# Kernel tuning notes

Hardware: AMD Instinct MI355X
Metric: run time of the kernel (lower is better)

## Reference

```python
import jax, jax.numpy as jnp
import numpy as np

B, C, T, H = 2, 1024, 2048, 16
D = C // H  # head dim = 64


def setup_inputs() -> dict:
    key = jax.random.key(0)
    ks = jax.random.split(key, 10)
    s = 1.0 / np.sqrt(C).astype(np.float32)
    x = jax.random.normal(ks[0], (B, C, T), jnp.float32)
    mask = jax.random.randint(ks[1], (B, 1, T), 0, 2).astype(bool)
    Wq = jax.random.normal(ks[2], (C, C), jnp.float32) * s
    bq = jax.random.normal(ks[3], (C,), jnp.float32) * 0.02
    Wk = jax.random.normal(ks[4], (C, C), jnp.float32) * s
    bk = jax.random.normal(ks[5], (C,), jnp.float32) * 0.02
    Wv = jax.random.normal(ks[6], (C, C), jnp.float32) * s
    bv = jax.random.normal(ks[7], (C,), jnp.float32) * 0.02
    Wp = jax.random.normal(ks[8], (C, C), jnp.float32) * s
    bp = jax.random.normal(ks[9], (C,), jnp.float32) * 0.02
    return {"x": x, "mask": mask, "Wq": Wq, "bq": bq, "Wk": Wk, "bk": bk,
            "Wv": Wv, "bv": bv, "Wp": Wp, "bp": bp}


def _conv1x1(W, b, z):
    # Conv1d with kernel size 1 == per-position GEMM over channels.
    return jnp.einsum('oc,bct->bot', W, z) + b[None, :, None]


def reference(x, mask, Wq, bq, Wk, bk, Wv, bv, Wp, bp):
    b_, c_, t_ = x.shape
    scale = 1.0 / np.sqrt(D).astype(np.float32)
    q = _conv1x1(Wq, bq, x)
    k = _conv1x1(Wk, bk, x)
    v = _conv1x1(Wv, bv, x)
    # [B, C, T] -> [B, H, T, D]  (view(B,H,D,T).transpose(2,3))
    q = q.reshape(b_, H, D, t_).transpose(0, 1, 3, 2)
    k = k.reshape(b_, H, D, t_).transpose(0, 1, 3, 2)
    v = v.reshape(b_, H, D, t_).transpose(0, 1, 3, 2)
    att = jnp.einsum('bhqd,bhkd->bhqk', q * scale, k)
    m = mask[:, :, None, :]  # [B,1,1,T] key mask
    att = jnp.where(m, att, -jnp.inf)
    p = jax.nn.softmax(att, axis=-1)
    p = jnp.where(m, p, 0.0)
    vm = v * mask[:, :, :, None].astype(v.dtype)  # zero masked values
    out = jnp.einsum('bhqk,bhkd->bhqd', p, vm)
    # [B,H,T,D] -> [B,C,T]
    out = out.transpose(0, 1, 3, 2).reshape(b_, c_, t_)
    out = _conv1x1(Wp, bp, out) * mask.astype(out.dtype)
    return (out, mask)
```

## Files before the change

### kernel.cpp

```cpp
#include <hip/hip_runtime.h>

typedef unsigned short u16;
typedef unsigned int u32;
typedef short bf16x8 __attribute__((ext_vector_type(8)));
typedef float f32x4 __attribute__((ext_vector_type(4)));

constexpr int Bb = 2, Cc = 1024, Tt = 2048, Hh = 16, Dd = 64;

__device__ __forceinline__ u16 f2bf(float f) {
    union { float f; u32 i; } c; c.f = f;
    u32 u = c.i;
    u32 r = (u + 0x7FFFu + ((u >> 16) & 1u)) >> 16;
    return (u16)r;
}
__device__ __forceinline__ u32 pk_bf2(float lo, float hi) {
    union { float f; u32 i; } a, b; a.f = lo; b.f = hi;
    u32 ua = a.i + 0x8000u, ub = b.i + 0x8000u;
    return (ub & 0xFFFF0000u) | (ua >> 16);
}
__device__ __forceinline__ u32 scl2(u32 w) {
    union { float f; u32 i; } lo, hi;
    lo.i = w << 16; hi.i = w & 0xFFFF0000u;
    lo.f *= 0.125f; hi.f *= 0.125f;
    return (hi.i & 0xFFFF0000u) | (lo.i >> 16);
}
__device__ __forceinline__ void gl_lds16(const u16* g, u16* l) {
    __builtin_amdgcn_global_load_lds(
        (const __attribute__((address_space(1))) u32*)(const void*)g,
        (__attribute__((address_space(3))) u32*)(void*)l, 16, 0, 0);
}

__global__ __launch_bounds__(256) void prep(const int* __restrict__ mask,
                                            int* __restrict__ pfx,
                                            int* __restrict__ tmap,
                                            int* __restrict__ nk,
                                            const float* __restrict__ w0,
                                            const float* __restrict__ w1,
                                            const float* __restrict__ w2,
                                            const float* __restrict__ w3,
                                            u16* __restrict__ wout) {
    if (blockIdx.x < 2) {
        __shared__ int part[256];
        int b = blockIdx.x;
        const int* m = mask + b * Tt;
        int t8 = threadIdx.x * 8;
        int v[8], s = 0;
#pragma unroll
        for (int i = 0; i < 8; i++) { v[i] = m[t8 + i] ? 1 : 0; s += v[i]; }
        part[threadIdx.x] = s;
        __syncthreads();
        for (int off = 1; off < 256; off <<= 1) {
            int val = (threadIdx.x >= off) ? part[threadIdx.x - off] : 0;
            __syncthreads();
            part[threadIdx.x] += val;
            __syncthreads();
        }
        int run = part[threadIdx.x] - s;
#pragma unroll
        for (int i = 0; i < 8; i++) {
            pfx[b * Tt + t8 + i] = run;
            if (v[i]) { tmap[b * Tt + run] = t8 + i; run++; }
        }
        if (threadIdx.x == 255) nk[b] = part[255];
    } else {
        int bi = blockIdx.x - 2;
        int wsel = bi >> 10, blk = bi & 1023;
        const float* in = (wsel == 0) ? w0 : (wsel == 1) ? w1 : (wsel == 2) ? w2 : w3;
        u16* o = wout + (size_t)wsel * Cc * Cc;
        int i = (blk * 256 + threadIdx.x) * 4;
        float4 v = *(const float4*)(in + i);
        o[i + 0] = f2bf(v.x);
        o[i + 1] = f2bf(v.y);
        o[i + 2] = f2bf(v.z);
        o[i + 3] = f2bf(v.w);
    }
}

__global__ __launch_bounds__(256) void transpose_x(const float* __restrict__ x,
                                                   const int* __restrict__ mask,
                                                   const int* __restrict__ pfx,
                                                   u16* __restrict__ xT) {
    __shared__ u16 tile[32][33];
    int b = blockIdx.z;
    int t0 = blockIdx.x * 32, c0 = blockIdx.y * 32;
    int tx = threadIdx.x, ty = threadIdx.y;
    const float* xb = x + (size_t)b * Cc * Tt;
    u16* xTb = xT + (size_t)b * Tt * Cc;
#pragma unroll
    for (int i = 0; i < 4; i++) {
        int r = ty + i * 8;
        tile[r][tx] = f2bf(xb[(size_t)(c0 + r) * Tt + t0 + tx]);
    }
    __syncthreads();
#pragma unroll
    for (int i = 0; i < 4; i++) {
        int r = ty + i * 8;
        int t = t0 + r;
        if (mask[b * Tt + t]) {
            int slot = pfx[b * Tt + t];
            xTb[(size_t)slot * Cc + c0 + tx] = tile[tx][r];
        }
    }
}

__global__ __launch_bounds__(256) void gemm_qkv(const u16* __restrict__ A,
                                                const u16* __restrict__ Bt,
                                                const float* __restrict__ b0,
                                                const float* __restrict__ b1,
                                                const float* __restrict__ b2,
                                                const int* __restrict__ nk,
                                                u16* __restrict__ qb, u16* __restrict__ kb,
                                                u16* __restrict__ vT) {
    constexpr int K = Cc;
    __shared__ u16 Alds[128 * 64];
    __shared__ u16 Blds[128 * 64];
    int n0 = blockIdx.x * 128, m0 = blockIdx.y * 128;
    int bb = m0 >> 11;
    if ((m0 & 2047) >= nk[bb]) return;
    int tid = threadIdx.x;
    int lane = tid & 63, wave = tid >> 6;
    int quad = lane >> 4, id15 = lane & 15;
    int wm0 = (wave & 1) * 64, wn0 = (wave >> 1) * 64;
    int srow = lane >> 3;
    int scol = ((lane & 7) ^ srow) * 8;
    int sw = id15 & 7;

    f32x4 acc[4][4] = {};

    for (int k0 = 0; k0 < K; k0 += 64) {
        __syncthreads();
#pragma unroll
        for (int t = 0; t < 4; t++) {
            int g = wave * 4 + t;
            int r = g * 8 + srow;
            gl_lds16(A + (size_t)(m0 + r) * K + k0 + scol, &Alds[g * 512]);
            gl_lds16(Bt + (size_t)(n0 + r) * K + k0 + scol, &Blds[g * 512]);
        }
        __syncthreads();
#pragma unroll
        for (int hf = 0; hf < 2; hf++) {
            bf16x8 af[4], bf[4];
#pragma unroll
            for (int i = 0; i < 4; i++) {
                int c = (((hf << 2) | quad) ^ sw) * 8;
                af[i] = *(const bf16x8*)(&Alds[(wm0 + i * 16 + id15) * 64 + c]);
                bf[i] = *(const bf16x8*)(&Blds[(wn0 + i * 16 + id15) * 64 + c]);
            }
#pragma unroll
            for (int ni = 0; ni < 4; ni++)
#pragma unroll
                for (int mi = 0; mi < 4; mi++)
                    acc[ni][mi] = __builtin_amdgcn_mfma_f32_16x16x32_bf16(
                        bf[ni], af[mi], acc[ni][mi], 0, 0, 0);
        }
    }

    int mt0 = (m0 & 2047) + wm0;
#pragma unroll
    for (int ni = 0; ni < 4; ni++) {
        int nr = n0 + wn0 + ni * 16 + quad * 4;
        int sect = nr >> 10;
        int nn = nr & 1023;
        int h = nn >> 6, d0 = nn & 63;
        const float* bp_ = (sect == 0) ? b0 : (sect == 1) ? b1 : b2;
        float4 bv4 = *(const float4*)(bp_ + nn);
        if (sect < 2) {
            u16* dst = ((sect == 0) ? qb : kb) + ((size_t)bb * Hh + h) * Tt * (size_t)Dd;
#pragma unroll
            for (int mi = 0; mi < 4; mi++) {
                int mt = mt0 + mi * 16 + id15;
                uint2 w;
                w.x = pk_bf2(acc[ni][mi][0] + bv4.x, acc[ni][mi][1] + bv4.y);
                w.y = pk_bf2(acc[ni][mi][2] + bv4.z, acc[ni][mi][3] + bv4.w);
                *(uint2*)(dst + (size_t)mt * Dd + d0) = w;
            }
        } else {
            u16* dst = vT + ((size_t)bb * Hh + h) * Dd * (size_t)Tt;
#pragma unroll
            for (int mi = 0; mi < 4; mi++) {
                int mt = mt0 + mi * 16 + id15;
                dst[(size_t)(d0 + 0) * Tt + mt] = f2bf(acc[ni][mi][0] + bv4.x);
                dst[(size_t)(d0 + 1) * Tt + mt] = f2bf(acc[ni][mi][1] + bv4.y);
                dst[(size_t)(d0 + 2) * Tt + mt] = f2bf(acc[ni][mi][2] + bv4.z);
                dst[(size_t)(d0 + 3) * Tt + mt] = f2bf(acc[ni][mi][3] + bv4.w);
            }
        }
    }
}

__global__ __launch_bounds__(256) void gemm_proj(const u16* __restrict__ A,
                                                 const u16* __restrict__ Bt,
                                                 const float* __restrict__ b0,
                                                 const int* __restrict__ mask,
                                                 float* __restrict__ out,
                                                 float* __restrict__ outTail) {
    constexpr int K = Cc;
    __shared__ u16 Alds[128 * 64];
    __shared__ u16 Blds[64 * 64];
    int n0 = blockIdx.x * 64, m0 = blockIdx.y * 128;
    int tid = threadIdx.x;
    if (outTail && blockIdx.x == 0 && blockIdx.y == 0) {
        for (int i = tid; i < Bb * Tt; i += 256) outTail[i] = mask[i] ? 1.0f : 0.0f;
    }
    int lane = tid & 63, wave = tid >> 6;
    int quad = lane >> 4, id15 = lane & 15;
    int wn0 = (wave & 1) * 32, wm0 = (wave >> 1) * 64;
    int srow = lane >> 3;
    int scol = ((lane & 7) ^ srow) * 8;
    int sw = id15 & 7;

    f32x4 acc[2][4] = {};

    for (int k0 = 0; k0 < K; k0 += 64) {
        __syncthreads();
#pragma unroll
        for (int t = 0; t < 4; t++) {
            int g = wave * 4 + t;
            gl_lds16(A + (size_t)(m0 + g * 8 + srow) * K + k0 + scol, &Alds[g * 512]);
        }
#pragma unroll
        for (int t = 0; t < 2; t++) {
            int g = wave * 2 + t;
            gl_lds16(Bt + (size_t)(n0 + g * 8 + srow) * K + k0 + scol, &Blds[g * 512]);
        }
        __syncthreads();
#pragma unroll
        for (int hf = 0; hf < 2; hf++) {
            bf16x8 af[4], bf[2];
            int c = (((hf << 2) | quad) ^ sw) * 8;
#pragma unroll
            for (int i = 0; i < 4; i++)
                af[i] = *(const bf16x8*)(&Alds[(wm0 + i * 16 + id15) * 64 + c]);
#pragma unroll
            for (int i = 0; i < 2; i++)
                bf[i] = *(const bf16x8*)(&Blds[(wn0 + i * 16 + id15) * 64 + c]);
#pragma unroll
            for (int ni = 0; ni < 2; ni++)
#pragma unroll
                for (int mi = 0; mi < 4; mi++)
                    acc[ni][mi] = __builtin_amdgcn_mfma_f32_16x16x32_bf16(
                        bf[ni], af[mi], acc[ni][mi], 0, 0, 0);
        }
    }

    int bb = m0 >> 11;
    int mt0 = (m0 & 2047) + wm0;
#pragma unroll
    for (int ni = 0; ni < 2; ni++) {
        int nr = n0 + wn0 + ni * 16 + quad * 4;
        float4 bv4 = *(const float4*)(b0 + nr);
#pragma unroll
        for (int mi = 0; mi < 4; mi++) {
            int m = mt0 + mi * 16 + id15;
            int mg = (bb << 11) + m;
            float mm = (float)mask[mg];
            float* o = out + ((size_t)bb * Cc + nr) * Tt + m;
            o[0 * Tt] = (acc[ni][mi][0] + bv4.x) * mm;
            o[1 * Tt] = (acc[ni][mi][1] + bv4.y) * mm;
            o[2 * Tt] = (acc[ni][mi][2] + bv4.z) * mm;
            o[3 * Tt] = (acc[ni][mi][3] + bv4.w) * mm;
        }
    }
}

__global__ __launch_bounds__(256) void attn(const u16* __restrict__ q,
                                            const u16* __restrict__ kk,
                                            const u16* __restrict__ vT,
                                            const int* __restrict__ tmap,
                                            const int* __restrict__ nk,
                                            u16* __restrict__ o_buf) {
    __shared__ u16 Kl[2][128 * 64];
    __shared__ u16 Vl[2][64 * 128];
    int bh = blockIdx.y;
    int b = bh >> 4, h = bh & 15;
    int t0 = blockIdx.x * 64;
    int nkb = nk[b];
    if (t0 >= nkb) return;
    int tid = threadIdx.x;
    int lane = tid & 63, wave = tid >> 6;
    int quad = lane >> 4, id15 = lane & 15;
    int wq = t0 + wave * 16;
    const u16* qb = q + (size_t)bh * Tt * Dd;
    const u16* kb = kk + (size_t)bh * Tt * Dd;
    const u16* vb = vT + (size_t)bh * Dd * Tt;

    union { uint4 r; bf16x8 v; } qf[2];
#pragma unroll
    for (int hf = 0; hf < 2; hf++) {
        uint4 r = *(const uint4*)(qb + (size_t)(wq + id15) * Dd + hf * 32 + quad * 8);
        qf[hf].r.x = scl2(r.x);
        qf[hf].r.y = scl2(r.y);
        qf[hf].r.z = scl2(r.z);
        qf[hf].r.w = scl2(r.w);
    }

    int srowK = lane >> 3;
    int scolK = ((lane & 7) ^ srowK) * 8;
    int srowV = lane >> 4;
    int sw = id15 & 7;

    float l = 0.0f;
    f32x4 accO[4] = {};

#pragma unroll
    for (int t = 0; t < 4; t++) {
        int g = wave * 4 + t;
        gl_lds16(kb + (size_t)(g * 8 + srowK) * Dd + scolK, &Kl[0][g * 512]);
        int d = g * 4 + srowV;
        int sc = (lane & 15) ^ (4 * (g & 1) + srowV);
        gl_lds16(vb + (size_t)d * Tt + sc * 8, &Vl[0][g * 512]);
    }

    int shA = ((quad & 1) * 2) * 16 + id15;
    int shB = shA + 16;

    int cbuf = 0;
    for (int j0 = 0; j0 < nkb; j0 += 128, cbuf ^= 1) {
        __syncthreads();
        if (j0 + 128 < nkb) {
            int bn = cbuf ^ 1, jn = j0 + 128;
#pragma unroll
            for (int t = 0; t < 4; t++) {
                int g = wave * 4 + t;
                gl_lds16(kb + (size_t)(jn + g * 8 + srowK) * Dd + scolK, &Kl[bn][g * 512]);
                int d = g * 4 + srowV;
                int sc = (lane & 15) ^ (4 * (g & 1) + srowV);
                gl_lds16(vb + (size_t)d * Tt + jn + sc * 8, &Vl[bn][g * 512]);
            }
        }
        const u16* Kb = Kl[cbuf];
        const u16* Vb = Vl[cbuf];

        f32x4 st[8] = {};
#pragma unroll
        for (int kt = 0; kt < 8; kt++) {
            int krow = kt * 16 + id15;
#pragma unroll
            for (int hf = 0; hf < 2; hf++) {
                bf16x8 kf = *(const bf16x8*)(Kb + krow * 64 + (((hf << 2) | quad) ^ sw) * 8);
                st[kt] = __builtin_amdgcn_mfma_f32_16x16x32_bf16(kf, qf[hf].v, st[kt], 0, 0, 0);
            }
        }

        if (j0 + 128 > nkb) {
#pragma unroll
            for (int kt = 0; kt < 8; kt++) {
                int jb = j0 + kt * 16 + quad * 4;
#pragma unroll
                for (int r = 0; r < 4; r++)
                    if (jb + r >= nkb) st[kt][r] = -1e30f;
            }
        }

        u32 pkk[4][2][2];
#pragma unroll
        for (int kt = 0; kt < 8; kt++) {
            float p0 = __expf(st[kt][0]);
            float p1 = __expf(st[kt][1]);
            float p2 = __expf(st[kt][2]);
            float p3 = __expf(st[kt][3]);
            l += (p0 + p1) + (p2 + p3);
            pkk[kt >> 1][kt & 1][0] = pk_bf2(p0, p1);
            pkk[kt >> 1][kt & 1][1] = pk_bf2(p2, p3);
        }

#pragma unroll
        for (int g = 0; g < 4; g++) {
            union { u32 u[4]; bf16x8 v; } pf;
            u32 a0 = (u32)__shfl((int)pkk[g][0][0], shA);
            u32 a1 = (u32)__shfl((int)pkk[g][0][1], shA);
            u32 a2 = (u32)__shfl((int)pkk[g][0][0], shB);
            u32 a3 = (u32)__shfl((int)pkk[g][0][1], shB);
            u32 c0 = (u32)__shfl((int)pkk[g][1][0], shA);
            u32 c1 = (u32)__shfl((int)pkk[g][1][1], shA);
            u32 c2 = (u32)__shfl((int)pkk[g][1][0], shB);
            u32 c3 = (u32)__shfl((int)pkk[g][1][1], shB);
            pf.u[0] = (quad < 2) ? a0 : c0;
            pf.u[1] = (quad < 2) ? a1 : c1;
            pf.u[2] = (quad < 2) ? a2 : c2;
            pf.u[3] = (quad < 2) ? a3 : c3;
#pragma unroll
            for (int dt = 0; dt < 4; dt++) {
                int drow = dt * 16 + id15;
                bf16x8 vf = *(const bf16x8*)(Vb + drow * 128 + (((g << 2) | quad) ^ sw) * 8);
                accO[dt] = __builtin_amdgcn_mfma_f32_16x16x32_bf16(vf, pf.v, accO[dt], 0, 0, 0);
            }
        }
    }

    int slot = wq + id15;
    bool ok = slot < nkb;
    int torig = ok ? tmap[b * Tt + slot] : 0;
    float lv = l;
    lv += __shfl_xor(lv, 16);
    lv += __shfl_xor(lv, 32);
    float inv = 1.0f / lv;
    if (ok) {
#pragma unroll
        for (int dt = 0; dt < 4; dt++) {
            uint2 w;
            w.x = pk_bf2(accO[dt][0] * inv, accO[dt][1] * inv);
            w.y = pk_bf2(accO[dt][2] * inv, accO[dt][3] * inv);
            *(uint2*)(o_buf + ((size_t)b * Tt + torig) * Cc + h * Dd + dt * 16 + quad * 4) = w;
        }
    }
}

extern "C" void kernel_launch(void* const* d_in, const int* in_sizes, int n_in,
                              void* d_out, int out_size, void* d_ws, size_t ws_size,
                              hipStream_t stream) {
    const float* x  = (const float*)d_in[0];
    const int* mask = (const int*)d_in[1];
    const float* Wq = (const float*)d_in[2];
    const float* bq = (const float*)d_in[3];
    const float* Wk = (const float*)d_in[4];
    const float* bk = (const float*)d_in[5];
    const float* Wv = (const float*)d_in[6];
    const float* bv = (const float*)d_in[7];
    const float* Wp = (const float*)d_in[8];
    const float* bp = (const float*)d_in[9];
    float* out = (float*)d_out;

    size_t sz = (size_t)Bb * Tt * Cc;
    size_t wsz = (size_t)Cc * Cc;
    u16* xT = (u16*)d_ws;
    u16* qb = xT + sz;
    u16* kb = qb + sz;
    u16* vT = kb + sz;
    u16* wq16 = vT + sz;
    u16* wp16 = wq16 + 3 * wsz;
    int* pfx  = (int*)(wp16 + wsz);
    int* tmap = pfx + Bb * Tt;
    int* nkp  = tmap + Bb * Tt;
    u16* ob = xT;

    float* outTail = (out_size >= Bb * Cc * Tt + Bb * Tt)
                         ? out + (size_t)Bb * Cc * Tt : nullptr;

    prep<<<2 + 4 * (int)(wsz / 1024), 256, 0, stream>>>(
        mask, pfx, tmap, nkp, Wq, Wk, Wv, Wp, wq16);
    transpose_x<<<dim3(Tt / 32, Cc / 32, Bb), dim3(32, 8), 0, stream>>>(x, mask, pfx, xT);
    gemm_qkv<<<dim3(3 * Cc / 128, Bb * Tt / 128), 256, 0, stream>>>(
        xT, wq16, bq, bk, bv, nkp, qb, kb, vT);
    attn<<<dim3(Tt / 64, Bb * Hh), 256, 0, stream>>>(qb, kb, vT, tmap, nkp, ob);
    gemm_proj<<<dim3(Cc / 64, Bb * Tt / 128), 256, 0, stream>>>(
        ob, wp16, bp, mask, out, outTail);
}
```

Baseline: 186.6 us.

## Shrink GEMM M-tiles and split attention keys across waves for more blocks

Both GEMMs now use 64-row M tiles instead of 128, which doubles the grid size and halves per-wave accumulator work. The attention kernel now handles 32 queries per block and splits the key range into two halves processed by separate wave pairs. The two partial results are merged through LDS before the output is normalised. The aim is more blocks and better CU occupancy for a small problem. In exchange, the attention loop drops K/V double-buffering (loads now stall on syncs), each block redoes more Q/K/V loading, and the split-key merge adds extra syncs.

```diff
diff --git a/kernel.cpp b/kernel.cpp
--- a/kernel.cpp
+++ b/kernel.cpp
@@ -112,44 +112,48 @@
                                                 u16* __restrict__ qb, u16* __restrict__ kb,
                                                 u16* __restrict__ vT) {
     constexpr int K = Cc;
-    __shared__ u16 Alds[128 * 64];
+    __shared__ u16 Alds[64 * 64];
     __shared__ u16 Blds[128 * 64];
-    int n0 = blockIdx.x * 128, m0 = blockIdx.y * 128;
+    int n0 = blockIdx.x * 128, m0 = blockIdx.y * 64;
     int bb = m0 >> 11;
     if ((m0 & 2047) >= nk[bb]) return;
     int tid = threadIdx.x;
     int lane = tid & 63, wave = tid >> 6;
     int quad = lane >> 4, id15 = lane & 15;
-    int wm0 = (wave & 1) * 64, wn0 = (wave >> 1) * 64;
-    int srow = lane >> 3;
-    int scol = ((lane & 7) ^ srow) * 8;
+    int wm0 = (wave & 1) * 32, wn0 = (wave >> 1) * 64;
     int sw = id15 & 7;
 
-    f32x4 acc[4][4] = {};
+    f32x4 acc[4][2] = {};
 
     for (int k0 = 0; k0 < K; k0 += 64) {
         __syncthreads();
 #pragma unroll
-        for (int t = 0; t < 4; t++) {
-            int g = wave * 4 + t;
-            int r = g * 8 + srow;
-            gl_lds16(A + (size_t)(m0 + r) * K + k0 + scol, &Alds[g * 512]);
-            gl_lds16(Bt + (size_t)(n0 + r) * K + k0 + scol, &Blds[g * 512]);
+        for (int i = 0; i < 2; i++) {
+            int s = wave * 128 + i * 64 + lane;
+            int r = s >> 3, c = (s & 7) ^ (r & 7);
+            gl_lds16(A + (size_t)(m0 + r) * K + k0 + c * 8, &Alds[(wave * 128 + i * 64) * 8]);
+        }
+#pragma unroll
+        for (int i = 0; i < 4; i++) {
+            int s = wave * 256 + i * 64 + lane;
+            int r = s >> 3, c = (s & 7) ^ (r & 7);
+            gl_lds16(Bt + (size_t)(n0 + r) * K + k0 + c * 8, &Blds[(wave * 256 + i * 64) * 8]);
         }
         __syncthreads();
 #pragma unroll
         for (int hf = 0; hf < 2; hf++) {
-            bf16x8 af[4], bf[4];
-#pragma unroll
-            for (int i = 0; i < 4; i++) {
-                int c = (((hf << 2) | quad) ^ sw) * 8;
-                af[i] = *(const bf16x8*)(&Alds[(wm0 + i * 16 + id15) * 64 + c]);
-                bf[i] = *(const bf16x8*)(&Blds[(wn0 + i * 16 + id15) * 64 + c]);
-            }
+            int cc = (((hf << 2) | quad) ^ sw) * 8;
+            bf16x8 af[2], bf[4];
+#pragma unroll
+            for (int mi = 0; mi < 2; mi++)
+                af[mi] = *(const bf16x8*)(&Alds[(wm0 + mi * 16 + id15) * 64 + cc]);
 #pragma unroll
             for (int ni = 0; ni < 4; ni++)
-#pragma unroll
-                for (int mi = 0; mi < 4; mi++)
+                bf[ni] = *(const bf16x8*)(&Blds[(wn0 + ni * 16 + id15) * 64 + cc]);
+#pragma unroll
+            for (int ni = 0; ni < 4; ni++)
+#pragma unroll
+                for (int mi = 0; mi < 2; mi++)
                     acc[ni][mi] = __builtin_amdgcn_mfma_f32_16x16x32_bf16(
                         bf[ni], af[mi], acc[ni][mi], 0, 0, 0);
         }
@@ -167,7 +171,7 @@
         if (sect < 2) {
             u16* dst = ((sect == 0) ? qb : kb) + ((size_t)bb * Hh + h) * Tt * (size_t)Dd;
 #pragma unroll
-            for (int mi = 0; mi < 4; mi++) {
+            for (int mi = 0; mi < 2; mi++) {
                 int mt = mt0 + mi * 16 + id15;
                 uint2 w;
                 w.x = pk_bf2(acc[ni][mi][0] + bv4.x, acc[ni][mi][1] + bv4.y);
@@ -177,7 +181,7 @@
         } else {
             u16* dst = vT + ((size_t)bb * Hh + h) * Dd * (size_t)Tt;
 #pragma unroll
-            for (int mi = 0; mi < 4; mi++) {
+            for (int mi = 0; mi < 2; mi++) {
                 int mt = mt0 + mi * 16 + id15;
                 dst[(size_t)(d0 + 0) * Tt + mt] = f2bf(acc[ni][mi][0] + bv4.x);
                 dst[(size_t)(d0 + 1) * Tt + mt] = f2bf(acc[ni][mi][1] + bv4.y);
@@ -195,49 +199,43 @@
                                                  float* __restrict__ out,
                                                  float* __restrict__ outTail) {
     constexpr int K = Cc;
-    __shared__ u16 Alds[128 * 64];
+    __shared__ u16 Alds[64 * 64];
     __shared__ u16 Blds[64 * 64];
-    int n0 = blockIdx.x * 64, m0 = blockIdx.y * 128;
+    int n0 = blockIdx.x * 64, m0 = blockIdx.y * 64;
     int tid = threadIdx.x;
     if (outTail && blockIdx.x == 0 && blockIdx.y == 0) {
         for (int i = tid; i < Bb * Tt; i += 256) outTail[i] = mask[i] ? 1.0f : 0.0f;
     }
     int lane = tid & 63, wave = tid >> 6;
     int quad = lane >> 4, id15 = lane & 15;
-    int wn0 = (wave & 1) * 32, wm0 = (wave >> 1) * 64;
-    int srow = lane >> 3;
-    int scol = ((lane & 7) ^ srow) * 8;
+    int wn0 = (wave & 1) * 32, wm0 = (wave >> 1) * 32;
     int sw = id15 & 7;
 
-    f32x4 acc[2][4] = {};
+    f32x4 acc[2][2] = {};
 
     for (int k0 = 0; k0 < K; k0 += 64) {
         __syncthreads();
 #pragma unroll
-        for (int t = 0; t < 4; t++) {
-            int g = wave * 4 + t;
-            gl_lds16(A + (size_t)(m0 + g * 8 + srow) * K + k0 + scol, &Alds[g * 512]);
-        }
-#pragma unroll
-        for (int t = 0; t < 2; t++) {
-            int g = wave * 2 + t;
-            gl_lds16(Bt + (size_t)(n0 + g * 8 + srow) * K + k0 + scol, &Blds[g * 512]);
+        for (int i = 0; i < 2; i++) {
+            int s = wave * 128 + i * 64 + lane;
+            int r = s >> 3, c = (s & 7) ^ (r & 7);
+            gl_lds16(A + (size_t)(m0 + r) * K + k0 + c * 8, &Alds[(wave * 128 + i * 64) * 8]);
+            gl_lds16(Bt + (size_t)(n0 + r) * K + k0 + c * 8, &Blds[(wave * 128 + i * 64) * 8]);
         }
         __syncthreads();
 #pragma unroll
         for (int hf = 0; hf < 2; hf++) {
-            bf16x8 af[4], bf[2];
-            int c = (((hf << 2) | quad) ^ sw) * 8;
-#pragma unroll
-            for (int i = 0; i < 4; i++)
-                af[i] = *(const bf16x8*)(&Alds[(wm0 + i * 16 + id15) * 64 + c]);
-#pragma unroll
-            for (int i = 0; i < 2; i++)
-                bf[i] = *(const bf16x8*)(&Blds[(wn0 + i * 16 + id15) * 64 + c]);
+            int cc = (((hf << 2) | quad) ^ sw) * 8;
+            bf16x8 af[2], bf[2];
+#pragma unroll
+            for (int i = 0; i < 2; i++) {
+                af[i] = *(const bf16x8*)(&Alds[(wm0 + i * 16 + id15) * 64 + cc]);
+                bf[i] = *(const bf16x8*)(&Blds[(wn0 + i * 16 + id15) * 64 + cc]);
+            }
 #pragma unroll
             for (int ni = 0; ni < 2; ni++)
 #pragma unroll
-                for (int mi = 0; mi < 4; mi++)
+                for (int mi = 0; mi < 2; mi++)
                     acc[ni][mi] = __builtin_amdgcn_mfma_f32_16x16x32_bf16(
                         bf[ni], af[mi], acc[ni][mi], 0, 0, 0);
         }
@@ -250,7 +248,7 @@
         int nr = n0 + wn0 + ni * 16 + quad * 4;
         float4 bv4 = *(const float4*)(b0 + nr);
 #pragma unroll
-        for (int mi = 0; mi < 4; mi++) {
+        for (int mi = 0; mi < 2; mi++) {
             int m = mt0 + mi * 16 + id15;
             int mg = (bb << 11) + m;
             float mm = (float)mask[mg];
@@ -269,17 +267,18 @@
                                             const int* __restrict__ tmap,
                                             const int* __restrict__ nk,
                                             u16* __restrict__ o_buf) {
-    __shared__ u16 Kl[2][128 * 64];
-    __shared__ u16 Vl[2][64 * 128];
+    __shared__ u16 Kl[2][64 * 64];
+    __shared__ u16 Vl[2][64 * 64];
     int bh = blockIdx.y;
     int b = bh >> 4, h = bh & 15;
-    int t0 = blockIdx.x * 64;
+    int t0 = blockIdx.x * 32;
     int nkb = nk[b];
     if (t0 >= nkb) return;
     int tid = threadIdx.x;
     int lane = tid & 63, wave = tid >> 6;
     int quad = lane >> 4, id15 = lane & 15;
-    int wq = t0 + wave * 16;
+    int qg = wave & 1, kh = wave >> 1;
+    int wq = t0 + qg * 16;
     const u16* qb = q + (size_t)bh * Tt * Dd;
     const u16* kb = kk + (size_t)bh * Tt * Dd;
     const u16* vb = vT + (size_t)bh * Dd * Tt;
@@ -294,57 +293,50 @@
         qf[hf].r.w = scl2(r.w);
     }
 
-    int srowK = lane >> 3;
-    int scolK = ((lane & 7) ^ srowK) * 8;
-    int srowV = lane >> 4;
-    int sw = id15 & 7;
+    int nch = (nkb + 63) >> 6;
+    int nch0 = (nch + 1) >> 1;
+    int koff = kh ? nch0 * 64 : 0;
+    int kend = kh ? nkb : ((nch0 * 64 < nkb) ? nch0 * 64 : nkb);
 
     float l = 0.0f;
     f32x4 accO[4] = {};
-
-#pragma unroll
-    for (int t = 0; t < 4; t++) {
-        int g = wave * 4 + t;
-        gl_lds16(kb + (size_t)(g * 8 + srowK) * Dd + scolK, &Kl[0][g * 512]);
-        int d = g * 4 + srowV;
-        int sc = (lane & 15) ^ (4 * (g & 1) + srowV);
-        gl_lds16(vb + (size_t)d * Tt + sc * 8, &Vl[0][g * 512]);
-    }
-
     int shA = ((quad & 1) * 2) * 16 + id15;
     int shB = shA + 16;
-
-    int cbuf = 0;
-    for (int j0 = 0; j0 < nkb; j0 += 128, cbuf ^= 1) {
-        __syncthreads();
-        if (j0 + 128 < nkb) {
-            int bn = cbuf ^ 1, jn = j0 + 128;
-#pragma unroll
-            for (int t = 0; t < 4; t++) {
-                int g = wave * 4 + t;
-                gl_lds16(kb + (size_t)(jn + g * 8 + srowK) * Dd + scolK, &Kl[bn][g * 512]);
-                int d = g * 4 + srowV;
-                int sc = (lane & 15) ^ (4 * (g & 1) + srowV);
-                gl_lds16(vb + (size_t)d * Tt + jn + sc * 8, &Vl[bn][g * 512]);
-            }
-        }
-        const u16* Kb = Kl[cbuf];
-        const u16* Vb = Vl[cbuf];
-
-        f32x4 st[8] = {};
-#pragma unroll
-        for (int kt = 0; kt < 8; kt++) {
+    const u16* Kb = Kl[kh];
+    const u16* Vb = Vl[kh];
+
+    for (int c = 0; c < nch0; c++) {
+        int j0 = koff + c * 64;
+        bool live = j0 < kend;
+        __syncthreads();
+        if (live) {
+#pragma unroll
+            for (int i = 0; i < 4; i++) {
+                int s = qg * 256 + i * 64 + lane;
+                int r = s >> 3, cc = (s & 7) ^ (r & 7);
+                gl_lds16(kb + (size_t)(j0 + r) * Dd + cc * 8,
+                         &Kl[kh][(qg * 256 + i * 64) * 8]);
+                gl_lds16(vb + (size_t)r * Tt + j0 + cc * 8,
+                         &Vl[kh][(qg * 256 + i * 64) * 8]);
+            }
+        }
+        __syncthreads();
+        if (!live) continue;
+
+        f32x4 st[4] = {};
+#pragma unroll
+        for (int kt = 0; kt < 4; kt++) {
             int krow = kt * 16 + id15;
 #pragma unroll
             for (int hf = 0; hf < 2; hf++) {
-                bf16x8 kf = *(const bf16x8*)(Kb + krow * 64 + (((hf << 2) | quad) ^ sw) * 8);
+                bf16x8 kf = *(const bf16x8*)(Kb + krow * 64 +
+                                             (((hf << 2) | quad) ^ (krow & 7)) * 8);
                 st[kt] = __builtin_amdgcn_mfma_f32_16x16x32_bf16(kf, qf[hf].v, st[kt], 0, 0, 0);
             }
         }
-
-        if (j0 + 128 > nkb) {
-#pragma unroll
-            for (int kt = 0; kt < 8; kt++) {
+        if (j0 + 64 > nkb) {
+#pragma unroll
+            for (int kt = 0; kt < 4; kt++) {
                 int jb = j0 + kt * 16 + quad * 4;
 #pragma unroll
                 for (int r = 0; r < 4; r++)
@@ -352,9 +344,9 @@
             }
         }
 
-        u32 pkk[4][2][2];
-#pragma unroll
-        for (int kt = 0; kt < 8; kt++) {
+        u32 pkk[2][2][2];
+#pragma unroll
+        for (int kt = 0; kt < 4; kt++) {
             float p0 = __expf(st[kt][0]);
             float p1 = __expf(st[kt][1]);
             float p2 = __expf(st[kt][2]);
@@ -365,7 +357,7 @@
         }
 
 #pragma unroll
-        for (int g = 0; g < 4; g++) {
+        for (int g = 0; g < 2; g++) {
             union { u32 u[4]; bf16x8 v; } pf;
             u32 a0 = (u32)__shfl((int)pkk[g][0][0], shA);
             u32 a1 = (u32)__shfl((int)pkk[g][0][1], shA);
@@ -382,26 +374,45 @@
 #pragma unroll
             for (int dt = 0; dt < 4; dt++) {
                 int drow = dt * 16 + id15;
-                bf16x8 vf = *(const bf16x8*)(Vb + drow * 128 + (((g << 2) | quad) ^ sw) * 8);
+                bf16x8 vf = *(const bf16x8*)(Vb + drow * 64 +
+                                             (((g << 2) | quad) ^ (drow & 7)) * 8);
                 accO[dt] = __builtin_amdgcn_mfma_f32_16x16x32_bf16(vf, pf.v, accO[dt], 0, 0, 0);
             }
         }
     }
 
-    int slot = wq + id15;
-    bool ok = slot < nkb;
-    int torig = ok ? tmap[b * Tt + slot] : 0;
-    float lv = l;
-    lv += __shfl_xor(lv, 16);
-    lv += __shfl_xor(lv, 32);
-    float inv = 1.0f / lv;
-    if (ok) {
-#pragma unroll
-        for (int dt = 0; dt < 4; dt++) {
-            uint2 w;
-            w.x = pk_bf2(accO[dt][0] * inv, accO[dt][1] * inv);
-            w.y = pk_bf2(accO[dt][2] * inv, accO[dt][3] * inv);
-            *(uint2*)(o_buf + ((size_t)b * Tt + torig) * Cc + h * Dd + dt * 16 + quad * 4) = w;
+    __syncthreads();
+    float* mb = (float*)&Kl[0][0];
+    int base = (qg * 64 + lane) * 17;
+    if (kh == 1) {
+#pragma unroll
+        for (int dt = 0; dt < 4; dt++)
+#pragma unroll
+            for (int r = 0; r < 4; r++) mb[base + dt * 4 + r] = accO[dt][r];
+        mb[base + 16] = l;
+    }
+    __syncthreads();
+    if (kh == 0) {
+#pragma unroll
+        for (int dt = 0; dt < 4; dt++)
+#pragma unroll
+            for (int r = 0; r < 4; r++) accO[dt][r] += mb[base + dt * 4 + r];
+        l += mb[base + 16];
+        l += __shfl_xor(l, 16);
+        l += __shfl_xor(l, 32);
+        float inv = 1.0f / l;
+        int slot = wq + id15;
+        bool ok = slot < nkb;
+        int torig = ok ? tmap[b * Tt + slot] : 0;
+        if (ok) {
+#pragma unroll
+            for (int dt = 0; dt < 4; dt++) {
+                uint2 w;
+                w.x = pk_bf2(accO[dt][0] * inv, accO[dt][1] * inv);
+                w.y = pk_bf2(accO[dt][2] * inv, accO[dt][3] * inv);
+                *(uint2*)(o_buf + ((size_t)b * Tt + torig) * Cc + h * Dd +
+                          dt * 16 + quad * 4) = w;
+            }
         }
     }
 }
@@ -440,9 +451,9 @@
     prep<<<2 + 4 * (int)(wsz / 1024), 256, 0, stream>>>(
         mask, pfx, tmap, nkp, Wq, Wk, Wv, Wp, wq16);
     transpose_x<<<dim3(Tt / 32, Cc / 32, Bb), dim3(32, 8), 0, stream>>>(x, mask, pfx, xT);
-    gemm_qkv<<<dim3(3 * Cc / 128, Bb * Tt / 128), 256, 0, stream>>>(
+    gemm_qkv<<<dim3(3 * Cc / 128, Bb * Tt / 64), 256, 0, stream>>>(
         xT, wq16, bq, bk, bv, nkp, qb, kb, vT);
-    attn<<<dim3(Tt / 64, Bb * Hh), 256, 0, stream>>>(qb, kb, vT, tmap, nkp, ob);
-    gemm_proj<<<dim3(Cc / 64, Bb * Tt / 128), 256, 0, stream>>>(
+    attn<<<dim3(Tt / 32, Bb * Hh), 256, 0, stream>>>(qb, kb, vT, tmap, nkp, ob);
+    gemm_proj<<<dim3(Cc / 64, Bb * Tt / 64), 256, 0, stream>>>(
         ob, wp16, bp, mask, out, outTail);
 }
```

After: 184.6 us. About the same (-1.1%).
